# Performance work log

Hardware: AMD Instinct MI355X
Metric: run time of the kernel (lower is better)

The kernel has to match this reference:

```python
import jax, jax.numpy as jnp
import numpy as np

N_AGENTS, RNN_H, N_HEADS, GAT_D, EMB, SDIM = 16, 64, 4, 32, 32, 128


def setup_inputs() -> dict:
    key = jax.random.key(0)
    ks = jax.random.split(key, 16)
    xav = lambda k, shp: jax.random.normal(k, shp, jnp.float32) * (2.0 / sum(shp)) ** 0.5
    return {
        'agent_qs': jax.random.normal(ks[0], (32, 128, N_AGENTS), jnp.float32),
        'states': jax.random.normal(ks[1], (32, 128, SDIM), jnp.float32),
        'hidden_states': jax.random.normal(ks[2], (32, 128, N_AGENTS, RNN_H), jnp.float32),
        'uncertainty': jax.random.uniform(ks[3], (32, 128, 1), jnp.float32),
        'W_gat': xav(ks[4], (RNN_H, N_HEADS * GAT_D)) * 1.414,
        'att_a': xav(ks[5], (1, N_HEADS, 2 * GAT_D)) * 1.414,
        'w1s_W': xav(ks[6], (SDIM + 1, N_HEADS * EMB * GAT_D)),
        'w1s_b': jnp.zeros((N_HEADS * EMB * GAT_D,), jnp.float32),
        'b1_W': xav(ks[7], (SDIM, EMB)),
        'b1_b': jnp.zeros((EMB,), jnp.float32),
        'wf_W': xav(ks[8], (SDIM, EMB)),
        'wf_b': jnp.zeros((EMB,), jnp.float32),
        'V1_W': xav(ks[9], (SDIM, EMB)),
        'V1_b': jnp.zeros((EMB,), jnp.float32),
        'V2_W': xav(ks[10], (EMB, 1)),
        'V2_b': jnp.zeros((1,), jnp.float32),
    }


def gat(h, W_gat, att_a):
    B, n, _ = h.shape
    hp = (h @ W_gat).reshape(B, n, N_HEADS, GAT_D).transpose(0, 2, 1, 3)  # (B,H,n,d)
    a_src, a_dst = att_a[0, :, :GAT_D], att_a[0, :, GAT_D:]  # (H,d) each
    # e[b,h,i,j] = <hp_i, a_src> + <hp_j, a_dst>  (same math as concat+dot)
    src = jnp.einsum('bhnd,hd->bhn', hp, a_src)
    dst = jnp.einsum('bhnd,hd->bhn', hp, a_dst)
    e = jax.nn.leaky_relu(src[:, :, :, None] + dst[:, :, None, :], 0.2)
    attn = jax.nn.softmax(e, axis=-1)
    return jax.nn.elu(jnp.einsum('bhij,bhjd->bhid', attn, hp))  # (B,H,n,d)


def reference(agent_qs, states, hidden_states, uncertainty, W_gat, att_a,
              w1s_W, w1s_b, b1_W, b1_b, wf_W, wf_b, V1_W, V1_b, V2_W, V2_b):
    bs = agent_qs.shape[0]
    s = states.reshape(-1, SDIM)                      # (B,S)
    qs = agent_qs.reshape(-1, 1, N_AGENTS)            # (B,1,n)
    hs = hidden_states.reshape(-1, N_AGENTS, RNN_H)   # (B,n,R)
    unc = uncertainty.reshape(-1, 1)
    s_aug = jnp.concatenate([s, unc], axis=1)         # (B,S+1)

    g = gat(hs, W_gat, att_a)                         # (B,H,n,d)

    w1_state = (s_aug @ w1s_W + w1s_b).reshape(-1, N_HEADS, EMB, GAT_D)
    w1_heads = jnp.abs(jnp.einsum('bhed,bhnd->bhen', w1_state, g))  # (B,H,E,n)
    w1 = w1_heads.mean(axis=1).transpose(0, 2, 1)     # (B,n,E)

    b1 = (s @ b1_W + b1_b)[:, None, :]                # (B,1,E)
    hidden = jax.nn.elu(jnp.einsum('bin,bne->bie', qs, w1) + b1)  # (B,1,E)

    w_final = jnp.abs(s @ wf_W + wf_b)[:, :, None]    # (B,E,1)
    v = (jax.nn.relu(s @ V1_W + V1_b) @ V2_W + V2_b)[:, None, :]  # (B,1,1)
    y = jnp.einsum('bie,bej->bij', hidden, w_final) + v
    return y.reshape(bs, -1, 1)
```

## Files before the change

kernel.cpp:

```cpp
#include <hip/hip_runtime.h>
#include <hip/hip_bf16.h>
#include <math.h>


typedef __attribute__((ext_vector_type(8))) short short8;
typedef __attribute__((ext_vector_type(8))) unsigned short ushort8;
typedef __attribute__((ext_vector_type(4))) float float4v;
typedef __attribute__((ext_vector_type(4))) _Float16 half4v;

static __device__ inline unsigned short f2bf(float f) {
    unsigned int x;
    __builtin_memcpy(&x, &f, 4);
    unsigned int r = x + 0x7fffu + ((x >> 16) & 1u);
    return (unsigned short)(r >> 16);
}

static __device__ inline unsigned int cvtpk(float lo, float hi) {
    __hip_bfloat162 h = __float22bfloat162_rn(make_float2(lo, hi));
    unsigned int u;
    __builtin_memcpy(&u, &h, 4);
    return u;
}

static __device__ inline short8 pack8(float4 f0, float4 f1) {
    unsigned int u[4] = {cvtpk(f0.x, f0.y), cvtpk(f0.z, f0.w),
                         cvtpk(f1.x, f1.y), cvtpk(f1.z, f1.w)};
    short8 s;
    __builtin_memcpy(&s, u, 16);
    return s;
}

__global__ __launch_bounds__(256) void k0_prep(
    const float* __restrict__ w1s_W,
    const float* __restrict__ W_gat,
    const float* __restrict__ att_a,
    const float* __restrict__ states,
    const float* __restrict__ b1_W, const float* __restrict__ b1_b,
    const float* __restrict__ wf_W, const float* __restrict__ wf_b,
    const float* __restrict__ V1_W, const float* __restrict__ V1_b,
    const float* __restrict__ V2_W, const float* __restrict__ V2_b,
    unsigned short* __restrict__ w1sTf,
    unsigned short* __restrict__ WgTf,
    unsigned short* __restrict__ Sbf,
    float* __restrict__ b1v, float* __restrict__ wfv,
    float* __restrict__ out)
{
    __shared__ __align__(16) char SMEM[26112];
    const int tid = threadIdx.x, bx = blockIdx.x;

    if (bx < 256) {
        unsigned short* T = (unsigned short*)SMEM;
        const int c0 = bx * 16;
        const int cc = tid & 15, kr = tid >> 4;
        #pragma unroll
        for (int t = 0; t < 8; ++t) {
            int k = t * 16 + kr;
            T[cc * 136 + k] = f2bf(w1s_W[(size_t)k * 4096 + c0 + cc]);
        }
        __syncthreads();
        const int ks = tid >> 6, q = (tid >> 4) & 3, mm = tid & 15;
        *(ushort8*)&w1sTf[(size_t)bx * 2048 + tid * 8] =
            *(const ushort8*)&T[mm * 136 + ks * 32 + q * 8];
    } else if (bx == 256) {
        unsigned short* T = (unsigned short*)SMEM;
        #pragma unroll
        for (int t = 0; t < 32; ++t) {
            int i = t * 256 + tid;
            int k = i >> 7, c = i & 127;
            T[c * 72 + k] = f2bf(W_gat[k * 128 + c]);
        }
        __syncthreads();
        #pragma unroll
        for (int t = 0; t < 4; ++t) {
            int i = t * 256 + tid;
            int nt = i >> 7, w = i & 127;
            int kh = w >> 6, q = (w >> 4) & 3, mm = w & 15;
            *(ushort8*)&WgTf[nt * 1024 + w * 8] =
                *(const ushort8*)&T[(nt * 16 + mm) * 72 + kh * 32 + q * 8];
        }
        {
            const int k = tid >> 2, h = tid & 3;
            float ss = 0.f, dd = 0.f;
            #pragma unroll
            for (int d = 0; d < 32; ++d) {
                float wv = W_gat[k * 128 + h * 32 + d];
                ss = fmaf(wv, att_a[h * 64 + d], ss);
                dd = fmaf(wv, att_a[h * 64 + 32 + d], dd);
            }
            const int base = 8192 + (k >> 5) * 512 + ((k >> 3) & 3) * 128 + (k & 7);
            WgTf[base + h * 8]       = f2bf(ss);
            WgTf[base + (4 + h) * 8] = f2bf(dd);
        }
        #pragma unroll
        for (int t = 0; t < 2; ++t) {
            int i = t * 256 + tid;
            int kh = i >> 8, q = (i >> 6) & 3, mm = 8 + ((i >> 3) & 7), j = i & 7;
            WgTf[8192 + kh * 512 + q * 128 + mm * 8 + j] = 0;
        }
    } else {
        unsigned short* WLu = (unsigned short*)SMEM;
        for (int i = tid; i < 12288; i += 256) {
            float v = (i < 4096) ? b1_W[i] : (i < 8192 ? wf_W[i - 4096] : V1_W[i - 8192]);
            int set = i >> 12, k = (i >> 5) & 127, e = i & 31;
            WLu[set * 4352 + k * 34 + e] = f2bf(v);
        }
        __syncthreads();

        const int wave = tid >> 6, lane = tid & 63, mm = lane & 15, q = lane >> 4;
        const int b0w = (bx - 257) * 64 + wave * 16;

        short8 a[4];
        #pragma unroll
        for (int ks = 0; ks < 4; ++ks) {
            const float* sp = states + (size_t)(b0w + mm) * 128 + ks * 32 + q * 8;
            a[ks] = pack8(*(const float4*)sp, *(const float4*)(sp + 4));
        }
        #pragma unroll
        for (int ks = 0; ks < 4; ++ks)
            *(short8*)&Sbf[(size_t)(b0w + mm) * 128 + ks * 32 + q * 8] = a[ks];

        float4v accT[6];
        #pragma unroll
        for (int nt = 0; nt < 6; ++nt) accT[nt] = (float4v){0.f, 0.f, 0.f, 0.f};
        #pragma unroll
        for (int nt = 0; nt < 6; ++nt) {
            const int set = nt >> 1, e = (nt & 1) * 16 + mm;
            #pragma unroll
            for (int ks = 0; ks < 4; ++ks) {
                ushort8 bfu;
                #pragma unroll
                for (int j = 0; j < 8; ++j)
                    bfu[j] = WLu[set * 4352 + (ks * 32 + q * 8 + j) * 34 + e];
                short8 bf;
                __builtin_memcpy(&bf, &bfu, 16);
                accT[nt] = __builtin_amdgcn_mfma_f32_16x16x32_bf16(a[ks], bf, accT[nt], 0, 0, 0);
            }
        }
        float vsum[4] = {0.f, 0.f, 0.f, 0.f};
        #pragma unroll
        for (int p = 0; p < 2; ++p) {
            const int e = p * 16 + mm;
            const float bb1 = b1_b[e], bwf = wf_b[e], bv1 = V1_b[e], v2 = V2_W[e];
            #pragma unroll
            for (int reg = 0; reg < 4; ++reg) {
                const int row = b0w + q * 4 + reg;
                b1v[(size_t)row * 32 + e] = accT[p][reg] + bb1;
                wfv[(size_t)row * 32 + e] = fabsf(accT[2 + p][reg] + bwf);
                vsum[reg] += fmaxf(accT[4 + p][reg] + bv1, 0.f) * v2;
            }
        }
        #pragma unroll
        for (int reg = 0; reg < 4; ++reg) {
            vsum[reg] += __shfl_xor(vsum[reg], 1);
            vsum[reg] += __shfl_xor(vsum[reg], 2);
            vsum[reg] += __shfl_xor(vsum[reg], 4);
            vsum[reg] += __shfl_xor(vsum[reg], 8);
        }
        if (mm == 0) {
            #pragma unroll
            for (int reg = 0; reg < 4; ++reg)
                out[b0w + q * 4 + reg] = vsum[reg] + V2_b[0];
        }
    }
}

__global__ __launch_bounds__(256) void k2a_gemm(
    const unsigned short* __restrict__ w1sTf,
    const unsigned short* __restrict__ Sbf,
    const float* __restrict__ uncertainty,
    const float* __restrict__ w1s_W,
    const float* __restrict__ w1s_b,
    unsigned short* __restrict__ W2)
{
    __shared__ __align__(16) unsigned short Sb[64 * 136];
    const int bx = blockIdx.x;
    const int rb = bx >> 4, pg = bx & 15;
    const int tid = threadIdx.x;
    const int wave = tid >> 6, lane = tid & 63;
    const int m = lane & 15, quad = lane >> 4;

    {
        const int row = tid >> 2, seg = tid & 3;
        const unsigned short* src = &Sbf[(size_t)(rb * 64 + row) * 128 + seg * 32];
        #pragma unroll
        for (int k = 0; k < 4; ++k)
            *(ushort8*)&Sb[row * 136 + seg * 32 + k * 8] =
                *(const ushort8*)&src[k * 8];
    }

    const int E0 = pg * 8 + wave * 2;

    short8 A[2][2][4];
    #pragma unroll
    for (int e = 0; e < 2; ++e)
        #pragma unroll
        for (int t = 0; t < 2; ++t)
            #pragma unroll
            for (int ks = 0; ks < 4; ++ks)
                A[e][t][ks] = *(const short8*)&w1sTf[
                    (size_t)((E0 + e) * 2 + t) * 2048 + ks * 512 + lane * 8];

    const float* w128 = w1s_W + (size_t)128 * 4096;
    float wf[2][2][4], bb[2][2][4];
    #pragma unroll
    for (int e = 0; e < 2; ++e)
        #pragma unroll
        for (int t = 0; t < 2; ++t) {
            float4 w4 = *(const float4*)&w128[((E0 + e) * 2 + t) * 16 + quad * 4];
            float4 b4 = *(const float4*)&w1s_b[((E0 + e) * 2 + t) * 16 + quad * 4];
            wf[e][t][0] = w4.x; wf[e][t][1] = w4.y; wf[e][t][2] = w4.z; wf[e][t][3] = w4.w;
            bb[e][t][0] = b4.x; bb[e][t][1] = b4.y; bb[e][t][2] = b4.z; bb[e][t][3] = b4.w;
        }

    __syncthreads();

    #pragma unroll
    for (int c = 0; c < 4; ++c) {
        const int lr = c * 16 + m;
        const float us = uncertainty[rb * 64 + lr];
        short8 Bf[4];
        #pragma unroll
        for (int ks = 0; ks < 4; ++ks)
            Bf[ks] = *(const short8*)&Sb[lr * 136 + ks * 32 + quad * 8];

        float4v z[2][2];
        #pragma unroll
        for (int e = 0; e < 2; ++e)
            #pragma unroll
            for (int t = 0; t < 2; ++t)
                z[e][t] = (float4v){0.f, 0.f, 0.f, 0.f};
        #pragma unroll
        for (int ks = 0; ks < 4; ++ks)
            #pragma unroll
            for (int e = 0; e < 2; ++e)
                #pragma unroll
                for (int t = 0; t < 2; ++t)
                    z[e][t] = __builtin_amdgcn_mfma_f32_16x16x32_bf16(
                        A[e][t][ks], Bf[ks], z[e][t], 0, 0, 0);

        #pragma unroll
        for (int e = 0; e < 2; ++e) {
            const int E = E0 + e;
            unsigned int wpk[4];
            #pragma unroll
            for (int reg = 0; reg < 4; ++reg) {
                float za = z[e][0][reg] + us * wf[e][0][reg] + bb[e][0][reg];
                float zb = z[e][1][reg] + us * wf[e][1][reg] + bb[e][1][reg];
                wpk[reg] = cvtpk(za, zb);
            }
            short8 pk;
            __builtin_memcpy(&pk, wpk, 16);
            const int eo = (E >> 4) * 512 + (E & 15) * 32 + quad * 8;
            *(short8*)&W2[(size_t)(rb * 64 + lr) * 4096 + eo] = pk;
        }
    }
}

__global__ __launch_bounds__(256) void k1_gatmix(
    const float* __restrict__ hidden_states,
    const unsigned short* __restrict__ WgTf,
    const unsigned short* __restrict__ W2,
    const float* __restrict__ agent_qs,
    const float* __restrict__ b1v, const float* __restrict__ wfv,
    float* __restrict__ out)
{
    const int wave = threadIdx.x >> 6;
    const int b = blockIdx.x * 4 + wave;
    const int lane = threadIdx.x & 63, m = lane & 15, quad = lane >> 4;
    __shared__ __align__(16) float sc[4 * 320];
    float* scr = &sc[wave * 320];

    short8 wfr[8];
    #pragma unroll
    for (int i = 0; i < 8; ++i)
        wfr[i] = *(const short8*)&W2[(size_t)b * 4096 + i * 512 + m * 32 + quad * 8];
    const float qs_m = agent_qs[b * 16 + m];

    const float* hrow = hidden_states + ((size_t)b * 16 + m) * 64;
    float4 f0 = *(const float4*)(hrow + quad * 8);
    float4 f1 = *(const float4*)(hrow + quad * 8 + 4);
    short8 a0 = pack8(f0, f1);
    f0 = *(const float4*)(hrow + 32 + quad * 8);
    f1 = *(const float4*)(hrow + 32 + quad * 8 + 4);
    short8 a1 = pack8(f0, f1);

    float4v hpt[9];
    #pragma unroll
    for (int nt = 0; nt < 9; ++nt) {
        short8 bf0 = *(const short8*)&WgTf[nt * 1024 + lane * 8];
        short8 bf1 = *(const short8*)&WgTf[nt * 1024 + 512 + lane * 8];
        float4v z = (float4v){0.f, 0.f, 0.f, 0.f};
        z = __builtin_amdgcn_mfma_f32_16x16x32_bf16(a0, bf0, z, 0, 0, 0);
        z = __builtin_amdgcn_mfma_f32_16x16x32_bf16(a1, bf1, z, 0, 0, 0);
        hpt[nt] = z;
    }

    {
        float4 pr = {hpt[8][0], hpt[8][1], hpt[8][2], hpt[8][3]};
        *(float4*)&scr[m * 20 + quad * 4] = pr;
    }

    float Sacc[2][4] = {};

    #pragma unroll
    for (int h = 0; h < 4; ++h) {
        const float src_m = scr[h * 20 + m];
        float4 pdv = *(const float4*)&scr[(4 + h) * 20 + quad * 4];
        float pd[4] = {pdv.x, pdv.y, pdv.z, pdv.w};

        float e_[4];
        #pragma unroll
        for (int jj = 0; jj < 4; ++jj) {
            float x = src_m + pd[jj];
            e_[jj] = fmaxf(x, 0.2f * x);
        }
        float mx = fmaxf(fmaxf(e_[0], e_[1]), fmaxf(e_[2], e_[3]));
        mx = fmaxf(mx, __shfl_xor(mx, 16));
        mx = fmaxf(mx, __shfl_xor(mx, 32));
        float p_[4], ssum = 0.f;
        #pragma unroll
        for (int jj = 0; jj < 4; ++jj) { p_[jj] = __expf(e_[jj] - mx); ssum += p_[jj]; }
        ssum += __shfl_xor(ssum, 16);
        ssum += __shfl_xor(ssum, 32);
        const float inv = __builtin_amdgcn_rcpf(ssum);

        half4v bfrag;
        #pragma unroll
        for (int jj = 0; jj < 4; ++jj) bfrag[jj] = (_Float16)(p_[jj] * inv);

        float4v zp[2];
        #pragma unroll
        for (int p = 0; p < 2; ++p) {
            float4v ct = hpt[2 * h + p];
            half4v afrag;
            #pragma unroll
            for (int t = 0; t < 4; ++t) afrag[t] = (_Float16)ct[t];
            float4v z = (float4v){0.f, 0.f, 0.f, 0.f};
            zp[p] = __builtin_amdgcn_mfma_f32_16x16x16f16(afrag, bfrag, z, 0, 0, 0);
        }
        unsigned int w[4];
        #pragma unroll
        for (int t = 0; t < 4; ++t) {
            float x0 = zp[0][t];
            x0 = (x0 > 0.f) ? x0 : (__expf(x0) - 1.f);
            float x1 = zp[1][t];
            x1 = (x1 > 0.f) ? x1 : (__expf(x1) - 1.f);
            w[t] = cvtpk(x0, x1);
        }
        short8 gfrag;
        __builtin_memcpy(&gfrag, w, 16);

        #pragma unroll
        for (int H = 0; H < 2; ++H) {
            float4v z = (float4v){0.f, 0.f, 0.f, 0.f};
            z = __builtin_amdgcn_mfma_f32_16x16x32_bf16(wfr[h * 2 + H], gfrag, z, 0, 0, 0);
            #pragma unroll
            for (int reg = 0; reg < 4; ++reg)
                Sacc[H][reg] += fabsf(z[reg]);
        }
    }

    float local = 0.f;
    #pragma unroll
    for (int H = 0; H < 2; ++H) {
        float sn[4];
        #pragma unroll
        for (int reg = 0; reg < 4; ++reg) sn[reg] = Sacc[H][reg] * qs_m;
        #pragma unroll
        for (int mask = 1; mask <= 8; mask <<= 1) {
            #pragma unroll
            for (int reg = 0; reg < 4; ++reg) sn[reg] += __shfl_xor(sn[reg], mask);
        }
        float4 b4 = *(const float4*)&b1v[(size_t)b * 32 + H * 16 + quad * 4];
        float4 w4 = *(const float4*)&wfv[(size_t)b * 32 + H * 16 + quad * 4];
        float bq[4] = {b4.x, b4.y, b4.z, b4.w};
        float wq[4] = {w4.x, w4.y, w4.z, w4.w};
        #pragma unroll
        for (int reg = 0; reg < 4; ++reg) {
            float hid = 0.25f * sn[reg] + bq[reg];
            hid = (hid > 0.f) ? hid : expm1f(hid);
            local = fmaf(hid, wq[reg], local);
        }
    }
    local += __shfl_xor(local, 16);
    local += __shfl_xor(local, 32);
    if (lane == 0) out[b] = out[b] + local;
}

extern "C" void kernel_launch(void* const* d_in, const int* in_sizes, int n_in,
                              void* d_out, int out_size, void* d_ws, size_t ws_size,
                              hipStream_t stream)
{
    const float* agent_qs      = (const float*)d_in[0];
    const float* states        = (const float*)d_in[1];
    const float* hidden_states = (const float*)d_in[2];
    const float* uncertainty   = (const float*)d_in[3];
    const float* W_gat         = (const float*)d_in[4];
    const float* att_a         = (const float*)d_in[5];
    const float* w1s_W         = (const float*)d_in[6];
    const float* w1s_b         = (const float*)d_in[7];
    const float* b1_W          = (const float*)d_in[8];
    const float* b1_b          = (const float*)d_in[9];
    const float* wf_W          = (const float*)d_in[10];
    const float* wf_b          = (const float*)d_in[11];
    const float* V1_W          = (const float*)d_in[12];
    const float* V1_b          = (const float*)d_in[13];
    const float* V2_W          = (const float*)d_in[14];
    const float* V2_b          = (const float*)d_in[15];

    char* w = (char*)d_ws;
    unsigned short* w1sTf   = (unsigned short*)w;  w += (size_t)524288 * 2;
    unsigned short* WgTf    = (unsigned short*)w;  w += (size_t)9216 * 2;
    unsigned short* Sbf     = (unsigned short*)w;  w += (size_t)524288 * 2;
    unsigned short* W2      = (unsigned short*)w;  w += (size_t)16777216 * 2;
    float* b1v              = (float*)w;           w += (size_t)131072 * 4;
    float* wfv              = (float*)w;           w += (size_t)131072 * 4;
    float* out              = (float*)d_out;

    k0_prep<<<321, 256, 0, stream>>>(w1s_W, W_gat, att_a, states,
                                     b1_W, b1_b, wf_W, wf_b, V1_W, V1_b,
                                     V2_W, V2_b, w1sTf, WgTf, Sbf, b1v, wfv, out);

    k2a_gemm<<<1024, 256, 0, stream>>>(w1sTf, Sbf, uncertainty, w1s_W, w1s_b, W2);

    k1_gatmix<<<1024, 256, 0, stream>>>(hidden_states, WgTf, W2, agent_qs,
                                        b1v, wfv, out);
}
```

Measured before the change: 125.5 us.

## Split weight packing from prep and fuse state GEMM with small-head prep

Result: no change. 126.6 us (+0.9%).

```diff
diff --git a/kernel.cpp b/kernel.cpp
--- a/kernel.cpp
+++ b/kernel.cpp
@@ -30,38 +30,191 @@
     return s;
 }
 
-__global__ __launch_bounds__(256) void k0_prep(
+__global__ __launch_bounds__(256) void k0_pack(
     const float* __restrict__ w1s_W,
+    unsigned short* __restrict__ w1sTf)
+{
+    __shared__ __align__(16) unsigned short T[16 * 136];
+    const int tid = threadIdx.x, bx = blockIdx.x;
+    const int c0 = bx * 16;
+    const int cc = tid & 15, kr = tid >> 4;
+    #pragma unroll
+    for (int t = 0; t < 8; ++t) {
+        int k = t * 16 + kr;
+        T[cc * 136 + k] = f2bf(w1s_W[(size_t)k * 4096 + c0 + cc]);
+    }
+    __syncthreads();
+    const int ks = tid >> 6, q = (tid >> 4) & 3, mm = tid & 15;
+    *(ushort8*)&w1sTf[(size_t)bx * 2048 + tid * 8] =
+        *(const ushort8*)&T[mm * 136 + ks * 32 + q * 8];
+}
+
+__global__ __launch_bounds__(256) void kB_fused(
+    const unsigned short* __restrict__ w1sTf,
+    const float* __restrict__ states,
+    const float* __restrict__ uncertainty,
+    const float* __restrict__ w1s_W,
+    const float* __restrict__ w1s_b,
     const float* __restrict__ W_gat,
     const float* __restrict__ att_a,
-    const float* __restrict__ states,
     const float* __restrict__ b1_W, const float* __restrict__ b1_b,
     const float* __restrict__ wf_W, const float* __restrict__ wf_b,
     const float* __restrict__ V1_W, const float* __restrict__ V1_b,
     const float* __restrict__ V2_W, const float* __restrict__ V2_b,
-    unsigned short* __restrict__ w1sTf,
     unsigned short* __restrict__ WgTf,
-    unsigned short* __restrict__ Sbf,
+    unsigned short* __restrict__ W2,
     float* __restrict__ b1v, float* __restrict__ wfv,
     float* __restrict__ out)
 {
     __shared__ __align__(16) char SMEM[26112];
     const int tid = threadIdx.x, bx = blockIdx.x;
-
-    if (bx < 256) {
-        unsigned short* T = (unsigned short*)SMEM;
-        const int c0 = bx * 16;
-        const int cc = tid & 15, kr = tid >> 4;
-        #pragma unroll
-        for (int t = 0; t < 8; ++t) {
-            int k = t * 16 + kr;
-            T[cc * 136 + k] = f2bf(w1s_W[(size_t)k * 4096 + c0 + cc]);
-        }
+    const int wave = tid >> 6, lane = tid & 63;
+    const int m = lane & 15, quad = lane >> 4;
+
+    if (bx < 1024) {
+        unsigned short* Sb = (unsigned short*)SMEM;
+        const int rb = bx >> 4, pg = bx & 15;
+
+        {
+            const int row = tid >> 2, seg = tid & 3;
+            const float* src = &states[(size_t)(rb * 64 + row) * 128 + seg * 32];
+            #pragma unroll
+            for (int kk = 0; kk < 4; ++kk) {
+                float4 fa = *(const float4*)&src[kk * 8];
+                float4 fb = *(const float4*)&src[kk * 8 + 4];
+                unsigned int u[4] = {cvtpk(fa.x, fa.y), cvtpk(fa.z, fa.w),
+                                     cvtpk(fb.x, fb.y), cvtpk(fb.z, fb.w)};
+                __builtin_memcpy(&Sb[row * 136 + seg * 32 + kk * 8], u, 16);
+            }
+        }
+
+        const int E0 = pg * 8 + wave * 2;
+
+        short8 A[2][2][4];
+        #pragma unroll
+        for (int e = 0; e < 2; ++e)
+            #pragma unroll
+            for (int t = 0; t < 2; ++t)
+                #pragma unroll
+                for (int ks = 0; ks < 4; ++ks)
+                    A[e][t][ks] = *(const short8*)&w1sTf[
+                        (size_t)((E0 + e) * 2 + t) * 2048 + ks * 512 + lane * 8];
+
+        const float* w128 = w1s_W + (size_t)128 * 4096;
+        float wf[2][2][4], bb[2][2][4];
+        #pragma unroll
+        for (int e = 0; e < 2; ++e)
+            #pragma unroll
+            for (int t = 0; t < 2; ++t) {
+                float4 w4 = *(const float4*)&w128[((E0 + e) * 2 + t) * 16 + quad * 4];
+                float4 b4 = *(const float4*)&w1s_b[((E0 + e) * 2 + t) * 16 + quad * 4];
+                wf[e][t][0] = w4.x; wf[e][t][1] = w4.y; wf[e][t][2] = w4.z; wf[e][t][3] = w4.w;
+                bb[e][t][0] = b4.x; bb[e][t][1] = b4.y; bb[e][t][2] = b4.z; bb[e][t][3] = b4.w;
+            }
+
         __syncthreads();
-        const int ks = tid >> 6, q = (tid >> 4) & 3, mm = tid & 15;
-        *(ushort8*)&w1sTf[(size_t)bx * 2048 + tid * 8] =
-            *(const ushort8*)&T[mm * 136 + ks * 32 + q * 8];
-    } else if (bx == 256) {
+
+        #pragma unroll
+        for (int c = 0; c < 4; ++c) {
+            const int lr = c * 16 + m;
+            const float us = uncertainty[rb * 64 + lr];
+            short8 Bf[4];
+            #pragma unroll
+            for (int ks = 0; ks < 4; ++ks)
+                Bf[ks] = *(const short8*)&Sb[lr * 136 + ks * 32 + quad * 8];
+
+            float4v z[2][2];
+            #pragma unroll
+            for (int e = 0; e < 2; ++e)
+                #pragma unroll
+                for (int t = 0; t < 2; ++t)
+                    z[e][t] = (float4v){0.f, 0.f, 0.f, 0.f};
+            #pragma unroll
+            for (int ks = 0; ks < 4; ++ks)
+                #pragma unroll
+                for (int e = 0; e < 2; ++e)
+                    #pragma unroll
+                    for (int t = 0; t < 2; ++t)
+                        z[e][t] = __builtin_amdgcn_mfma_f32_16x16x32_bf16(
+                            A[e][t][ks], Bf[ks], z[e][t], 0, 0, 0);
+
+            #pragma unroll
+            for (int e = 0; e < 2; ++e) {
+                const int E = E0 + e;
+                unsigned int wpk[4];
+                #pragma unroll
+                for (int reg = 0; reg < 4; ++reg) {
+                    float za = z[e][0][reg] + us * wf[e][0][reg] + bb[e][0][reg];
+                    float zb = z[e][1][reg] + us * wf[e][1][reg] + bb[e][1][reg];
+                    wpk[reg] = cvtpk(za, zb);
+                }
+                short8 pk;
+                __builtin_memcpy(&pk, wpk, 16);
+                const int eo = (E >> 4) * 512 + (E & 15) * 32 + quad * 8;
+                *(short8*)&W2[(size_t)(rb * 64 + lr) * 4096 + eo] = pk;
+            }
+        }
+    } else if (bx < 1088) {
+        unsigned short* WLu = (unsigned short*)SMEM;
+        for (int i = tid; i < 12288; i += 256) {
+            float v = (i < 4096) ? b1_W[i] : (i < 8192 ? wf_W[i - 4096] : V1_W[i - 8192]);
+            int set = i >> 12, k = (i >> 5) & 127, e = i & 31;
+            WLu[set * 4352 + k * 34 + e] = f2bf(v);
+        }
+        __syncthreads();
+
+        const int b0w = (bx - 1024) * 64 + wave * 16;
+
+        short8 a[4];
+        #pragma unroll
+        for (int ks = 0; ks < 4; ++ks) {
+            const float* sp = states + (size_t)(b0w + m) * 128 + ks * 32 + quad * 8;
+            a[ks] = pack8(*(const float4*)sp, *(const float4*)(sp + 4));
+        }
+
+        float4v accT[6];
+        #pragma unroll
+        for (int nt = 0; nt < 6; ++nt) accT[nt] = (float4v){0.f, 0.f, 0.f, 0.f};
+        #pragma unroll
+        for (int nt = 0; nt < 6; ++nt) {
+            const int set = nt >> 1, e = (nt & 1) * 16 + m;
+            #pragma unroll
+            for (int ks = 0; ks < 4; ++ks) {
+                ushort8 bfu;
+                #pragma unroll
+                for (int j = 0; j < 8; ++j)
+                    bfu[j] = WLu[set * 4352 + (ks * 32 + quad * 8 + j) * 34 + e];
+                short8 bf;
+                __builtin_memcpy(&bf, &bfu, 16);
+                accT[nt] = __builtin_amdgcn_mfma_f32_16x16x32_bf16(a[ks], bf, accT[nt], 0, 0, 0);
+            }
+        }
+        float vsum[4] = {0.f, 0.f, 0.f, 0.f};
+        #pragma unroll
+        for (int p = 0; p < 2; ++p) {
+            const int e = p * 16 + m;
+            const float bb1 = b1_b[e], bwf = wf_b[e], bv1 = V1_b[e], v2 = V2_W[e];
+            #pragma unroll
+            for (int reg = 0; reg < 4; ++reg) {
+                const int row = b0w + quad * 4 + reg;
+                b1v[(size_t)row * 32 + e] = accT[p][reg] + bb1;
+                wfv[(size_t)row * 32 + e] = fabsf(accT[2 + p][reg] + bwf);
+                vsum[reg] += fmaxf(accT[4 + p][reg] + bv1, 0.f) * v2;
+            }
+        }
+        #pragma unroll
+        for (int reg = 0; reg < 4; ++reg) {
+            vsum[reg] += __shfl_xor(vsum[reg], 1);
+            vsum[reg] += __shfl_xor(vsum[reg], 2);
+            vsum[reg] += __shfl_xor(vsum[reg], 4);
+            vsum[reg] += __shfl_xor(vsum[reg], 8);
+        }
+        if (m == 0) {
+            #pragma unroll
+            for (int reg = 0; reg < 4; ++reg)
+                out[b0w + quad * 4 + reg] = vsum[reg] + V2_b[0];
+        }
+    } else {
         unsigned short* T = (unsigned short*)SMEM;
         #pragma unroll
         for (int t = 0; t < 32; ++t) {
@@ -94,164 +247,8 @@
         #pragma unroll
         for (int t = 0; t < 2; ++t) {
             int i = t * 256 + tid;
-            int kh = i >> 8, q = (i >> 6) & 3, mm = 8 + ((i >> 3) & 7), j = i & 7;
-            WgTf[8192 + kh * 512 + q * 128 + mm * 8 + j] = 0;
-        }
-    } else {
-        unsigned short* WLu = (unsigned short*)SMEM;
-        for (int i = tid; i < 12288; i += 256) {
-            float v = (i < 4096) ? b1_W[i] : (i < 8192 ? wf_W[i - 4096] : V1_W[i - 8192]);
-            int set = i >> 12, k = (i >> 5) & 127, e = i & 31;
-            WLu[set * 4352 + k * 34 + e] = f2bf(v);
-        }
-        __syncthreads();
-
-        const int wave = tid >> 6, lane = tid & 63, mm = lane & 15, q = lane >> 4;
-        const int b0w = (bx - 257) * 64 + wave * 16;
-
-        short8 a[4];
-        #pragma unroll
-        for (int ks = 0; ks < 4; ++ks) {
-            const float* sp = states + (size_t)(b0w + mm) * 128 + ks * 32 + q * 8;
-            a[ks] = pack8(*(const float4*)sp, *(const float4*)(sp + 4));
-        }
-        #pragma unroll
-        for (int ks = 0; ks < 4; ++ks)
-            *(short8*)&Sbf[(size_t)(b0w + mm) * 128 + ks * 32 + q * 8] = a[ks];
-
-        float4v accT[6];
-        #pragma unroll
-        for (int nt = 0; nt < 6; ++nt) accT[nt] = (float4v){0.f, 0.f, 0.f, 0.f};
-        #pragma unroll
-        for (int nt = 0; nt < 6; ++nt) {
-            const int set = nt >> 1, e = (nt & 1) * 16 + mm;
-            #pragma unroll
-            for (int ks = 0; ks < 4; ++ks) {
-                ushort8 bfu;
-                #pragma unroll
-                for (int j = 0; j < 8; ++j)
-                    bfu[j] = WLu[set * 4352 + (ks * 32 + q * 8 + j) * 34 + e];
-                short8 bf;
-                __builtin_memcpy(&bf, &bfu, 16);
-                accT[nt] = __builtin_amdgcn_mfma_f32_16x16x32_bf16(a[ks], bf, accT[nt], 0, 0, 0);
-            }
-        }
-        float vsum[4] = {0.f, 0.f, 0.f, 0.f};
-        #pragma unroll
-        for (int p = 0; p < 2; ++p) {
-            const int e = p * 16 + mm;
-            const float bb1 = b1_b[e], bwf = wf_b[e], bv1 = V1_b[e], v2 = V2_W[e];
-            #pragma unroll
-            for (int reg = 0; reg < 4; ++reg) {
-                const int row = b0w + q * 4 + reg;
-                b1v[(size_t)row * 32 + e] = accT[p][reg] + bb1;
-                wfv[(size_t)row * 32 + e] = fabsf(accT[2 + p][reg] + bwf);
-                vsum[reg] += fmaxf(accT[4 + p][reg] + bv1, 0.f) * v2;
-            }
-        }
-        #pragma unroll
-        for (int reg = 0; reg < 4; ++reg) {
-            vsum[reg] += __shfl_xor(vsum[reg], 1);
-            vsum[reg] += __shfl_xor(vsum[reg], 2);
-            vsum[reg] += __shfl_xor(vsum[reg], 4);
-            vsum[reg] += __shfl_xor(vsum[reg], 8);
-        }
-        if (mm == 0) {
-            #pragma unroll
-            for (int reg = 0; reg < 4; ++reg)
-                out[b0w + q * 4 + reg] = vsum[reg] + V2_b[0];
-        }
-    }
-}
-
-__global__ __launch_bounds__(256) void k2a_gemm(
-    const unsigned short* __restrict__ w1sTf,
-    const unsigned short* __restrict__ Sbf,
-    const float* __restrict__ uncertainty,
-    const float* __restrict__ w1s_W,
-    const float* __restrict__ w1s_b,
-    unsigned short* __restrict__ W2)
-{
-    __shared__ __align__(16) unsigned short Sb[64 * 136];
-    const int bx = blockIdx.x;
-    const int rb = bx >> 4, pg = bx & 15;
-    const int tid = threadIdx.x;
-    const int wave = tid >> 6, lane = tid & 63;
-    const int m = lane & 15, quad = lane >> 4;
-
-    {
-        const int row = tid >> 2, seg = tid & 3;
-        const unsigned short* src = &Sbf[(size_t)(rb * 64 + row) * 128 + seg * 32];
-        #pragma unroll
-        for (int k = 0; k < 4; ++k)
-            *(ushort8*)&Sb[row * 136 + seg * 32 + k * 8] =
-                *(const ushort8*)&src[k * 8];
-    }
-
-    const int E0 = pg * 8 + wave * 2;
-
-    short8 A[2][2][4];
-    #pragma unroll
-    for (int e = 0; e < 2; ++e)
-        #pragma unroll
-        for (int t = 0; t < 2; ++t)
-            #pragma unroll
-            for (int ks = 0; ks < 4; ++ks)
-                A[e][t][ks] = *(const short8*)&w1sTf[
-                    (size_t)((E0 + e) * 2 + t) * 2048 + ks * 512 + lane * 8];
-
-    const float* w128 = w1s_W + (size_t)128 * 4096;
-    float wf[2][2][4], bb[2][2][4];
-    #pragma unroll
-    for (int e = 0; e < 2; ++e)
-        #pragma unroll
-        for (int t = 0; t < 2; ++t) {
-            float4 w4 = *(const float4*)&w128[((E0 + e) * 2 + t) * 16 + quad * 4];
-            float4 b4 = *(const float4*)&w1s_b[((E0 + e) * 2 + t) * 16 + quad * 4];
-            wf[e][t][0] = w4.x; wf[e][t][1] = w4.y; wf[e][t][2] = w4.z; wf[e][t][3] = w4.w;
-            bb[e][t][0] = b4.x; bb[e][t][1] = b4.y; bb[e][t][2] = b4.z; bb[e][t][3] = b4.w;
-        }
-
-    __syncthreads();
-
-    #pragma unroll
-    for (int c = 0; c < 4; ++c) {
-        const int lr = c * 16 + m;
-        const float us = uncertainty[rb * 64 + lr];
-        short8 Bf[4];
-        #pragma unroll
-        for (int ks = 0; ks < 4; ++ks)
-            Bf[ks] = *(const short8*)&Sb[lr * 136 + ks * 32 + quad * 8];
-
-        float4v z[2][2];
-        #pragma unroll
-        for (int e = 0; e < 2; ++e)
-            #pragma unroll
-            for (int t = 0; t < 2; ++t)
-                z[e][t] = (float4v){0.f, 0.f, 0.f, 0.f};
-        #pragma unroll
-        for (int ks = 0; ks < 4; ++ks)
-            #pragma unroll
-            for (int e = 0; e < 2; ++e)
-                #pragma unroll
-                for (int t = 0; t < 2; ++t)
-                    z[e][t] = __builtin_amdgcn_mfma_f32_16x16x32_bf16(
-                        A[e][t][ks], Bf[ks], z[e][t], 0, 0, 0);
-
-        #pragma unroll
-        for (int e = 0; e < 2; ++e) {
-            const int E = E0 + e;
-            unsigned int wpk[4];
-            #pragma unroll
-            for (int reg = 0; reg < 4; ++reg) {
-                float za = z[e][0][reg] + us * wf[e][0][reg] + bb[e][0][reg];
-                float zb = z[e][1][reg] + us * wf[e][1][reg] + bb[e][1][reg];
-                wpk[reg] = cvtpk(za, zb);
-            }
-            short8 pk;
-            __builtin_memcpy(&pk, wpk, 16);
-            const int eo = (E >> 4) * 512 + (E & 15) * 32 + quad * 8;
-            *(short8*)&W2[(size_t)(rb * 64 + lr) * 4096 + eo] = pk;
+            int kh = i >> 8, q2 = (i >> 6) & 3, mm = 8 + ((i >> 3) & 7), j = i & 7;
+            WgTf[8192 + kh * 512 + q2 * 128 + mm * 8 + j] = 0;
         }
     }
 }
@@ -275,6 +272,12 @@
     for (int i = 0; i < 8; ++i)
         wfr[i] = *(const short8*)&W2[(size_t)b * 4096 + i * 512 + m * 32 + quad * 8];
     const float qs_m = agent_qs[b * 16 + m];
+    float4 b4h[2], w4h[2];
+    #pragma unroll
+    for (int H = 0; H < 2; ++H) {
+        b4h[H] = *(const float4*)&b1v[(size_t)b * 32 + H * 16 + quad * 4];
+        w4h[H] = *(const float4*)&wfv[(size_t)b * 32 + H * 16 + quad * 4];
+    }
 
     const float* hrow = hidden_states + ((size_t)b * 16 + m) * 64;
     float4 f0 = *(const float4*)(hrow + quad * 8);
@@ -371,10 +374,8 @@
             #pragma unroll
             for (int reg = 0; reg < 4; ++reg) sn[reg] += __shfl_xor(sn[reg], mask);
         }
-        float4 b4 = *(const float4*)&b1v[(size_t)b * 32 + H * 16 + quad * 4];
-        float4 w4 = *(const float4*)&wfv[(size_t)b * 32 + H * 16 + quad * 4];
-        float bq[4] = {b4.x, b4.y, b4.z, b4.w};
-        float wq[4] = {w4.x, w4.y, w4.z, w4.w};
+        float bq[4] = {b4h[H].x, b4h[H].y, b4h[H].z, b4h[H].w};
+        float wq[4] = {w4h[H].x, w4h[H].y, w4h[H].z, w4h[H].w};
         #pragma unroll
         for (int reg = 0; reg < 4; ++reg) {
             float hid = 0.25f * sn[reg] + bq[reg];
@@ -411,17 +412,17 @@
     char* w = (char*)d_ws;
     unsigned short* w1sTf   = (unsigned short*)w;  w += (size_t)524288 * 2;
     unsigned short* WgTf    = (unsigned short*)w;  w += (size_t)9216 * 2;
-    unsigned short* Sbf     = (unsigned short*)w;  w += (size_t)524288 * 2;
     unsigned short* W2      = (unsigned short*)w;  w += (size_t)16777216 * 2;
     float* b1v              = (float*)w;           w += (size_t)131072 * 4;
     float* wfv              = (float*)w;           w += (size_t)131072 * 4;
     float* out              = (float*)d_out;
 
-    k0_prep<<<321, 256, 0, stream>>>(w1s_W, W_gat, att_a, states,
-                                     b1_W, b1_b, wf_W, wf_b, V1_W, V1_b,
-                                     V2_W, V2_b, w1sTf, WgTf, Sbf, b1v, wfv, out);
-
-    k2a_gemm<<<1024, 256, 0, stream>>>(w1sTf, Sbf, uncertainty, w1s_W, w1s_b, W2);
+    k0_pack<<<256, 256, 0, stream>>>(w1s_W, w1sTf);
+
+    kB_fused<<<1089, 256, 0, stream>>>(w1sTf, states, uncertainty, w1s_W, w1s_b,
+                                       W_gat, att_a, b1_W, b1_b, wf_W, wf_b,
+                                       V1_W, V1_b, V2_W, V2_b,
+                                       WgTf, W2, b1v, wfv, out);
 
     k1_gatmix<<<1024, 256, 0, stream>>>(hidden_states, WgTf, W2, agent_qs,
                                         b1v, wfv, out);
```
